# Kernel tuning notes

Hardware: AMD Instinct MI355X
Metric: run time of the kernel (lower is better)

## Reference

```python
import jax, jax.numpy as jnp
import numpy as np

DIM = 512
BATCH, SEQ = 4, 4096


def setup_inputs() -> dict:
    key = jax.random.key(0)
    kx, kq, kk, kv, ko = jax.random.split(key, 5)
    s = DIM ** -0.5  # fan-in style init scale for stability
    return {
        "x": jax.random.normal(kx, (BATCH, SEQ, DIM), dtype=jnp.float32),
        "Wq": jax.random.normal(kq, (DIM, DIM), dtype=jnp.float32) * s,
        "Wk": jax.random.normal(kk, (DIM, DIM), dtype=jnp.float32) * s,
        "Wv": jax.random.normal(kv, (DIM, DIM), dtype=jnp.float32) * s,
        "Wo": jax.random.normal(ko, (DIM, DIM), dtype=jnp.float32) * s,
    }


def reference(x, Wq, Wk, Wv, Wo):
    # x: [B, S, D]; projections (torch Linear, no bias -> x @ W here)
    q = jnp.einsum('bsd,dk->bsk', x, Wq)  # [B,S,K]
    k = jnp.einsum('bsd,dk->bsk', x, Wk)  # [B,S,K]
    v = jnp.einsum('bsd,dv->bsv', x, Wv)  # [B,S,V]

    # sequential recurrence: M_t = M_{t-1} + v_t k_t^T ; y_t = M_t q_t
    def step(M, qkv_t):
        q_t, k_t, v_t = qkv_t  # each [B, K] / [B, V]
        M = M + v_t[:, :, None] * k_t[:, None, :]  # [B, V, K]
        y_t = jnp.einsum('bvk,bk->bv', M, q_t)
        return M, y_t

    M0 = jnp.zeros((x.shape[0], Wv.shape[1], Wk.shape[1]), dtype=x.dtype)
    qT = jnp.swapaxes(q, 0, 1)  # [S,B,K]
    kT = jnp.swapaxes(k, 0, 1)
    vT = jnp.swapaxes(v, 0, 1)
    _, ys = jax.lax.scan(step, M0, (qT, kT, vT))  # ys: [S,B,V]
    y = jnp.swapaxes(ys, 0, 1)  # [B,S,V]
    return jnp.einsum('bsv,vd->bsd', y, Wo)
```

## Files before the change

### kernel.cpp

```cpp
#include <hip/hip_runtime.h>
#include <hip/hip_bf16.h>

typedef __attribute__((ext_vector_type(8))) short bf16x8;
typedef __attribute__((ext_vector_type(4))) float f32x4;

__device__ inline short f2bf(float f) {
    __hip_bfloat16 h = __float2bfloat16(f);
    short s;
    __builtin_memcpy(&s, &h, 2);
    return s;
}
__device__ inline float bf2f(short s) {
    unsigned int u = ((unsigned int)(unsigned short)s) << 16;
    float f;
    __builtin_memcpy(&f, &u, 4);
    return f;
}

__device__ inline void cp16_async(const void* g, void* l) {
    __builtin_amdgcn_global_load_lds(
        (const __attribute__((address_space(1))) void*)g,
        (__attribute__((address_space(3))) void*)l, 16, 0, 0);
}

__global__ void prep_kernel(const float* __restrict__ x, short* __restrict__ Xb,
                            const float* __restrict__ W0, const float* __restrict__ W1,
                            const float* __restrict__ W2, const float* __restrict__ W3,
                            short* __restrict__ W4T) {
    __shared__ short sT[64][72];
    const int bid = blockIdx.x, tid = threadIdx.x;
    if (bid < 8192) {
        int i = bid * 256 + tid;
        float4 f = ((const float4*)x)[i];
        union { short s[4]; int2 v; } u;
        u.s[0] = f2bf(f.x); u.s[1] = f2bf(f.y); u.s[2] = f2bf(f.z); u.s[3] = f2bf(f.w);
        ((int2*)Xb)[i] = u.v;
        return;
    }
    const int wb = bid - 8192;
    const int w = wb >> 6, r = wb & 63;
    const int n0 = (r >> 3) * 64, k0 = (r & 7) * 64;
    const float* W = (w == 0) ? W0 : (w == 1) ? W1 : (w == 2) ? W2 : W3;
#pragma unroll
    for (int rr = 0; rr < 4; ++rr) {
        int c = rr * 256 + tid;
        int row = c >> 4, col4 = (c & 15) * 4;
        float4 f = *(const float4*)&W[(size_t)(k0 + row) * 512 + n0 + col4];
        sT[col4 + 0][row] = f2bf(f.x);
        sT[col4 + 1][row] = f2bf(f.y);
        sT[col4 + 2][row] = f2bf(f.z);
        sT[col4 + 3][row] = f2bf(f.w);
    }
    __syncthreads();
#pragma unroll
    for (int rr = 0; rr < 2; ++rr) {
        int c = rr * 256 + tid;
        int f = c >> 3, k8 = (c & 7) * 8;
        int4 v = *(const int4*)&sT[f][k8];
        *(int4*)&W4T[(size_t)w * 262144 + (size_t)(n0 + f) * 512 + k0 + k8] = v;
    }
}


#define LDS_DBUF __shared__ short sA[8192], sB[8192]

__device__ inline void mfma_kloop_dbuf(const short* __restrict__ A, int lda,
                                       const short* __restrict__ B, int ldb,
                                       int Kd, f32x4* acc,
                                       short* sA, short* sB) {
    const int tid = threadIdx.x, lane = tid & 63, wv = tid >> 6;
    const int quad = lane >> 4, lr = lane & 15;
    const int wr = (wv >> 1) * 64, wc = (wv & 1) * 64;
    const int c0 = tid, c1 = tid + 256;
    const int r0 = c0 >> 2, k80 = (c0 & 3) * 8;
    const int r1 = c1 >> 2, k81 = (c1 & 3) * 8;

    __syncthreads();
    cp16_async(A + (size_t)r0 * lda + k80, sA + c0 * 8);
    cp16_async(A + (size_t)r1 * lda + k81, sA + c1 * 8);
    cp16_async(B + (size_t)r0 * ldb + k80, sB + c0 * 8);
    cp16_async(B + (size_t)r1 * ldb + k81, sB + c1 * 8);

    int cur = 0;
    for (int k0 = 0; k0 < Kd; k0 += 32) {
        __syncthreads();
        const int nxt = cur ^ 1;
        if (k0 + 32 < Kd) {
            const short* An = A + k0 + 32;
            const short* Bn = B + k0 + 32;
            cp16_async(An + (size_t)r0 * lda + k80, sA + nxt * 4096 + c0 * 8);
            cp16_async(An + (size_t)r1 * lda + k81, sA + nxt * 4096 + c1 * 8);
            cp16_async(Bn + (size_t)r0 * ldb + k80, sB + nxt * 4096 + c0 * 8);
            cp16_async(Bn + (size_t)r1 * ldb + k81, sB + nxt * 4096 + c1 * 8);
        }
        const short* pa = sA + cur * 4096;
        const short* pb = sB + cur * 4096;
        bf16x8 af[4], bfr[4];
#pragma unroll
        for (int i = 0; i < 4; ++i)
            af[i] = *(const bf16x8*)&pa[(wr + i * 16 + lr) * 32 + quad * 8];
#pragma unroll
        for (int j = 0; j < 4; ++j)
            bfr[j] = *(const bf16x8*)&pb[(wc + j * 16 + lr) * 32 + quad * 8];
#pragma unroll
        for (int i = 0; i < 4; ++i)
#pragma unroll
            for (int j = 0; j < 4; ++j)
                acc[i * 4 + j] = __builtin_amdgcn_mfma_f32_16x16x32_bf16(af[i], bfr[j], acc[i * 4 + j], 0, 0, 0);
        cur = nxt;
    }
}

__device__ inline void store_out(float* p, float v) { *p = v; }
__device__ inline void store_out(short* p, float v) { *p = f2bf(v); }

template <typename OutT>
__device__ inline void store_tile128(OutT* C, int ldc, const f32x4* acc) {
    const int lane = threadIdx.x & 63, wv = threadIdx.x >> 6;
    const int quad = lane >> 4, lr = lane & 15;
    const int wr = (wv >> 1) * 64, wc = (wv & 1) * 64;
#pragma unroll
    for (int i = 0; i < 4; ++i)
#pragma unroll
        for (int j = 0; j < 4; ++j)
#pragma unroll
            for (int r = 0; r < 4; ++r)
                store_out(&C[(size_t)(wr + i * 16 + quad * 4 + r) * ldc + wc + j * 16 + lr],
                          acc[i * 4 + j][r]);
}

__global__ __launch_bounds__(256, 2) void proj_all(const short* __restrict__ Xb,
                                                   const short* __restrict__ W4T,
                                                   short* __restrict__ Qb, short* __restrict__ Kb,
                                                   short* __restrict__ Vt, short* __restrict__ Kt) {
    LDS_DBUF;
    f32x4 acc[16];
#pragma unroll
    for (int i = 0; i < 16; ++i) acc[i] = (f32x4){0.f, 0.f, 0.f, 0.f};
    const int bid = blockIdx.x;
    const int lane = threadIdx.x & 63, wv = threadIdx.x >> 6;
    const int quad = lane >> 4, lr = lane & 15;
    const int wr = (wv >> 1) * 64, wc = (wv & 1) * 64;
    if (bid < 1024) {
        const int mt = bid >> 3, by = bid & 7;
        const short* At = Xb + (size_t)mt * 128 * 512;
        const short* Bt = W4T + (size_t)by * 128 * 512;
        short* Ct = ((by < 4) ? Qb : Kb) + (size_t)mt * 128 * 512 + (by & 3) * 128;
        mfma_kloop_dbuf(At, 512, Bt, 512, 512, acc, sA, sB);
        store_tile128(Ct, 512, acc);
        if (by >= 4) {
            const int b = mt >> 5;
            const int t0b = (mt & 31) * 128;
            const int f0 = (by - 4) * 128;
#pragma unroll
            for (int i = 0; i < 4; ++i)
#pragma unroll
                for (int j = 0; j < 4; ++j) {
                    int f = f0 + wc + j * 16 + lr;
                    int tt0 = t0b + wr + i * 16 + quad * 4;
                    short tmp[4];
#pragma unroll
                    for (int r = 0; r < 4; ++r) tmp[r] = f2bf(acc[i * 4 + j][r]);
                    *(int2*)&Kt[((size_t)b * 512 + f) * 4096 + tt0] = *(const int2*)tmp;
                }
        }
    } else {
        const int r = bid - 1024;
        const int b = r & 3, tt = (r >> 2) & 31, ft = r >> 7;
        const short* At = W4T + (size_t)2 * 262144 + (size_t)ft * 128 * 512;
        const short* Bt = Xb + ((size_t)b * 4096 + tt * 128) * 512;
        short* Ct = Vt + (size_t)b * 512 * 4096 + (size_t)ft * 128 * 4096 + tt * 128;
        mfma_kloop_dbuf(At, 512, Bt, 512, 512, acc, sA, sB);
        store_tile128(Ct, 4096, acc);
    }
}

__global__ __launch_bounds__(256, 2) void phaseA_k(const short* __restrict__ Vt,
                                                   const short* __restrict__ Kt,
                                                   short* __restrict__ AM) {
    LDS_DBUF;
    const int vb = blockIdx.x;
    const int xt = vb & 3, yt = (vb >> 2) & 3, bc = vb >> 4;
    const int b = bc >> 4, c = bc & 15;
    const short* Ap = Vt + ((size_t)b * 512 + xt * 128) * 4096 + c * 256;
    const short* Bp = Kt + ((size_t)b * 512 + yt * 128) * 4096 + c * 256;
    short* Cp = AM + (size_t)bc * 262144 + (size_t)xt * 128 * 512 + yt * 128;
    f32x4 acc[16];
#pragma unroll
    for (int i = 0; i < 16; ++i) acc[i] = (f32x4){0.f, 0.f, 0.f, 0.f};
    mfma_kloop_dbuf(Ap, 4096, Bp, 4096, 256, acc, sA, sB);
    store_tile128(Cp, 512, acc);
}

__global__ __launch_bounds__(256, 2) void scan_phaseS_k(short* __restrict__ AM,
                                                        const short* __restrict__ Q,
                                                        const short* __restrict__ K,
                                                        short* __restrict__ P) {
    LDS_DBUF;
    const int tid = threadIdx.x;
    if (blockIdx.x < 512) {
        int i = blockIdx.x * 256 + tid;
        int b = i >> 15;
        int vk8 = i & 32767;
        size_t base = (size_t)b * 16 * 262144 + (size_t)vk8 * 8;
        float acc[8];
#pragma unroll
        for (int s = 0; s < 8; ++s) acc[s] = 0.f;
        for (int c = 0; c < 16; ++c) {
            short* p = AM + base + (size_t)c * 262144;
            short in8[8];
            *(int4*)in8 = *(const int4*)p;
            short out8[8];
#pragma unroll
            for (int s = 0; s < 8; ++s) out8[s] = f2bf(acc[s]);
            *(int4*)p = *(const int4*)out8;
#pragma unroll
            for (int s = 0; s < 8; ++s) acc[s] += bf2f(in8[s]);
        }
        return;
    }
    const int e = blockIdx.x - 512;
    const int bc = e >> 2, mt = e & 1, nt = (e >> 1) & 1;
    if (mt < nt) return;
    const int b = bc >> 4, c = bc & 15;
    short* Pt = P + (size_t)bc * 65536 + (size_t)mt * 128 * 256 + nt * 128;
    const short* Ap = Q + ((size_t)(b * 4096 + c * 256 + mt * 128)) * 512;
    const short* Bp = K + ((size_t)(b * 4096 + c * 256 + nt * 128)) * 512;
    f32x4 acc[16];
#pragma unroll
    for (int i = 0; i < 16; ++i) acc[i] = (f32x4){0.f, 0.f, 0.f, 0.f};
    mfma_kloop_dbuf(Ap, 512, Bp, 512, 512, acc, sA, sB);
    const int lane = tid & 63, wv = tid >> 6;
    const int quad = lane >> 4, lr = lane & 15;
    const int wr = (wv >> 1) * 64, wc = (wv & 1) * 64;
    const bool diag = (mt == nt);
#pragma unroll
    for (int i = 0; i < 4; ++i)
#pragma unroll
        for (int j = 0; j < 4; ++j)
#pragma unroll
            for (int r = 0; r < 4; ++r) {
                int t = wr + i * 16 + quad * 4 + r;
                int jj = wc + j * 16 + lr;
                float v = (!diag || jj <= t) ? acc[i * 4 + j][r] : 0.f;
                Pt[(size_t)t * 256 + jj] = f2bf(v);
            }
}

__global__ __launch_bounds__(256, 2) void phaseY_k(const short* __restrict__ Q,
                                                   const short* __restrict__ Mpre,
                                                   const short* __restrict__ P,
                                                   const short* __restrict__ Vt,
                                                   short* __restrict__ Y) {
    LDS_DBUF;
    const int vb = blockIdx.x;
    const int mt = vb & 1, nt = (vb >> 1) & 3, bc = vb >> 3;
    const int b = bc >> 4, c = bc & 15;
    f32x4 acc[16];
#pragma unroll
    for (int i = 0; i < 16; ++i) acc[i] = (f32x4){0.f, 0.f, 0.f, 0.f};
    const short* Ai = Q + ((size_t)(b * 4096 + c * 256 + mt * 128)) * 512;
    const short* Bi = Mpre + (size_t)bc * 262144 + (size_t)nt * 128 * 512;
    mfma_kloop_dbuf(Ai, 512, Bi, 512, 512, acc, sA, sB);
    const short* Ap = P + (size_t)bc * 65536 + (size_t)mt * 128 * 256;
    const short* Bv = Vt + ((size_t)b * 512 + nt * 128) * 4096 + c * 256;
    mfma_kloop_dbuf(Ap, 256, Bv, 4096, (mt + 1) * 128, acc, sA, sB);
    short* Cp = Y + ((size_t)(b * 4096 + c * 256 + mt * 128)) * 512 + nt * 128;
    store_tile128(Cp, 512, acc);
}

__global__ __launch_bounds__(256, 2) void outproj_k(const short* __restrict__ Y,
                                                    const short* __restrict__ W4T,
                                                    float* __restrict__ out) {
    LDS_DBUF;
    const int mt = blockIdx.x >> 2, nt = blockIdx.x & 3;
    const short* At = Y + (size_t)mt * 128 * 512;
    const short* Bt = W4T + (size_t)3 * 262144 + (size_t)nt * 128 * 512;
    float* Ct = out + (size_t)mt * 128 * 512 + nt * 128;
    f32x4 acc[16];
#pragma unroll
    for (int i = 0; i < 16; ++i) acc[i] = (f32x4){0.f, 0.f, 0.f, 0.f};
    mfma_kloop_dbuf(At, 512, Bt, 512, 512, acc, sA, sB);
    store_tile128(Ct, 512, acc);
}


extern "C" void kernel_launch(void* const* d_in, const int* in_sizes, int n_in,
                              void* d_out, int out_size, void* d_ws, size_t ws_size,
                              hipStream_t stream) {
    const float* x  = (const float*)d_in[0];
    const float* Wq = (const float*)d_in[1];
    const float* Wk = (const float*)d_in[2];
    const float* Wv = (const float*)d_in[3];
    const float* Wo = (const float*)d_in[4];
    float* out = (float*)d_out;

    const size_t NTD = 16384 * 512;

    short* ws  = (short*)d_ws;
    short* Xb  = ws;
    short* Qb  = Xb + NTD;
    short* Kb  = Qb + NTD;
    short* Kt  = Kb + NTD;
    short* Vt  = Kt + NTD;
    short* P   = Vt + NTD;
    short* W4T = P + 4194304;
    short* AM  = W4T + 1048576;
    short* Yb  = Kb;

    prep_kernel<<<8448, 256, 0, stream>>>(x, Xb, Wq, Wk, Wv, Wo, W4T);
    proj_all<<<1536, 256, 0, stream>>>(Xb, W4T, Qb, Kb, Vt, Kt);
    phaseA_k<<<1024, 256, 0, stream>>>(Vt, Kt, AM);
    scan_phaseS_k<<<768, 256, 0, stream>>>(AM, Qb, Kb, P);
    phaseY_k<<<512, 256, 0, stream>>>(Qb, AM, P, Vt, Yb);
    outproj_k<<<512, 256, 0, stream>>>(Yb, W4T, out);
}
```

Baseline: 233.9 us.

## Replace double-buffered K loop with four-panel 128-wide K staging

After: 237.6 us. About the same (+1.6%).

```diff
diff --git a/kernel.cpp b/kernel.cpp
--- a/kernel.cpp
+++ b/kernel.cpp
@@ -62,12 +62,12 @@
 }
 
 
-#define LDS_DBUF __shared__ short sA[8192], sB[8192]
-
-__device__ inline void mfma_kloop_dbuf(const short* __restrict__ A, int lda,
-                                       const short* __restrict__ B, int ldb,
-                                       int Kd, f32x4* acc,
-                                       short* sA, short* sB) {
+#define LDS_P4 __shared__ short sA[4][4096], sB[4][4096]
+
+__device__ inline void mfma_kloop128(const short* __restrict__ A, int lda,
+                                     const short* __restrict__ B, int ldb,
+                                     int Kd, f32x4* acc,
+                                     short (*sA)[4096], short (*sB)[4096]) {
     const int tid = threadIdx.x, lane = tid & 63, wv = tid >> 6;
     const int quad = lane >> 4, lr = lane & 15;
     const int wr = (wv >> 1) * 64, wc = (wv & 1) * 64;
@@ -75,39 +75,35 @@
     const int r0 = c0 >> 2, k80 = (c0 & 3) * 8;
     const int r1 = c1 >> 2, k81 = (c1 & 3) * 8;
 
-    __syncthreads();
-    cp16_async(A + (size_t)r0 * lda + k80, sA + c0 * 8);
-    cp16_async(A + (size_t)r1 * lda + k81, sA + c1 * 8);
-    cp16_async(B + (size_t)r0 * ldb + k80, sB + c0 * 8);
-    cp16_async(B + (size_t)r1 * ldb + k81, sB + c1 * 8);
-
-    int cur = 0;
-    for (int k0 = 0; k0 < Kd; k0 += 32) {
+    for (int k0 = 0; k0 < Kd; k0 += 128) {
         __syncthreads();
-        const int nxt = cur ^ 1;
-        if (k0 + 32 < Kd) {
-            const short* An = A + k0 + 32;
-            const short* Bn = B + k0 + 32;
-            cp16_async(An + (size_t)r0 * lda + k80, sA + nxt * 4096 + c0 * 8);
-            cp16_async(An + (size_t)r1 * lda + k81, sA + nxt * 4096 + c1 * 8);
-            cp16_async(Bn + (size_t)r0 * ldb + k80, sB + nxt * 4096 + c0 * 8);
-            cp16_async(Bn + (size_t)r1 * ldb + k81, sB + nxt * 4096 + c1 * 8);
+#pragma unroll
+        for (int p = 0; p < 4; ++p) {
+            const short* Apnl = A + k0 + p * 32;
+            const short* Bpnl = B + k0 + p * 32;
+            cp16_async(Apnl + (size_t)r0 * lda + k80, sA[p] + c0 * 8);
+            cp16_async(Apnl + (size_t)r1 * lda + k81, sA[p] + c1 * 8);
+            cp16_async(Bpnl + (size_t)r0 * ldb + k80, sB[p] + c0 * 8);
+            cp16_async(Bpnl + (size_t)r1 * ldb + k81, sB[p] + c1 * 8);
         }
-        const short* pa = sA + cur * 4096;
-        const short* pb = sB + cur * 4096;
-        bf16x8 af[4], bfr[4];
-#pragma unroll
-        for (int i = 0; i < 4; ++i)
-            af[i] = *(const bf16x8*)&pa[(wr + i * 16 + lr) * 32 + quad * 8];
-#pragma unroll
-        for (int j = 0; j < 4; ++j)
-            bfr[j] = *(const bf16x8*)&pb[(wc + j * 16 + lr) * 32 + quad * 8];
-#pragma unroll
-        for (int i = 0; i < 4; ++i)
+        __syncthreads();
+#pragma unroll
+        for (int p = 0; p < 4; ++p) {
+            const short* pa = sA[p];
+            const short* pb = sB[p];
+            bf16x8 af[4], bfr[4];
+#pragma unroll
+            for (int i = 0; i < 4; ++i)
+                af[i] = *(const bf16x8*)&pa[(wr + i * 16 + lr) * 32 + quad * 8];
 #pragma unroll
             for (int j = 0; j < 4; ++j)
-                acc[i * 4 + j] = __builtin_amdgcn_mfma_f32_16x16x32_bf16(af[i], bfr[j], acc[i * 4 + j], 0, 0, 0);
-        cur = nxt;
+                bfr[j] = *(const bf16x8*)&pb[(wc + j * 16 + lr) * 32 + quad * 8];
+#pragma unroll
+            for (int i = 0; i < 4; ++i)
+#pragma unroll
+                for (int j = 0; j < 4; ++j)
+                    acc[i * 4 + j] = __builtin_amdgcn_mfma_f32_16x16x32_bf16(af[i], bfr[j], acc[i * 4 + j], 0, 0, 0);
+        }
     }
 }
 
@@ -133,7 +129,7 @@
                                                    const short* __restrict__ W4T,
                                                    short* __restrict__ Qb, short* __restrict__ Kb,
                                                    short* __restrict__ Vt, short* __restrict__ Kt) {
-    LDS_DBUF;
+    LDS_P4;
     f32x4 acc[16];
 #pragma unroll
     for (int i = 0; i < 16; ++i) acc[i] = (f32x4){0.f, 0.f, 0.f, 0.f};
@@ -146,7 +142,7 @@
         const short* At = Xb + (size_t)mt * 128 * 512;
         const short* Bt = W4T + (size_t)by * 128 * 512;
         short* Ct = ((by < 4) ? Qb : Kb) + (size_t)mt * 128 * 512 + (by & 3) * 128;
-        mfma_kloop_dbuf(At, 512, Bt, 512, 512, acc, sA, sB);
+        mfma_kloop128(At, 512, Bt, 512, 512, acc, sA, sB);
         store_tile128(Ct, 512, acc);
         if (by >= 4) {
             const int b = mt >> 5;
@@ -170,7 +166,7 @@
         const short* At = W4T + (size_t)2 * 262144 + (size_t)ft * 128 * 512;
         const short* Bt = Xb + ((size_t)b * 4096 + tt * 128) * 512;
         short* Ct = Vt + (size_t)b * 512 * 4096 + (size_t)ft * 128 * 4096 + tt * 128;
-        mfma_kloop_dbuf(At, 512, Bt, 512, 512, acc, sA, sB);
+        mfma_kloop128(At, 512, Bt, 512, 512, acc, sA, sB);
         store_tile128(Ct, 4096, acc);
     }
 }
@@ -178,7 +174,7 @@
 __global__ __launch_bounds__(256, 2) void phaseA_k(const short* __restrict__ Vt,
                                                    const short* __restrict__ Kt,
                                                    short* __restrict__ AM) {
-    LDS_DBUF;
+    LDS_P4;
     const int vb = blockIdx.x;
     const int xt = vb & 3, yt = (vb >> 2) & 3, bc = vb >> 4;
     const int b = bc >> 4, c = bc & 15;
@@ -188,7 +184,7 @@
     f32x4 acc[16];
 #pragma unroll
     for (int i = 0; i < 16; ++i) acc[i] = (f32x4){0.f, 0.f, 0.f, 0.f};
-    mfma_kloop_dbuf(Ap, 4096, Bp, 4096, 256, acc, sA, sB);
+    mfma_kloop128(Ap, 4096, Bp, 4096, 256, acc, sA, sB);
     store_tile128(Cp, 512, acc);
 }
 
@@ -196,7 +192,7 @@
                                                         const short* __restrict__ Q,
                                                         const short* __restrict__ K,
                                                         short* __restrict__ P) {
-    LDS_DBUF;
+    LDS_P4;
     const int tid = threadIdx.x;
     if (blockIdx.x < 512) {
         int i = blockIdx.x * 256 + tid;
@@ -229,7 +225,7 @@
     f32x4 acc[16];
 #pragma unroll
     for (int i = 0; i < 16; ++i) acc[i] = (f32x4){0.f, 0.f, 0.f, 0.f};
-    mfma_kloop_dbuf(Ap, 512, Bp, 512, 512, acc, sA, sB);
+    mfma_kloop128(Ap, 512, Bp, 512, 512, acc, sA, sB);
     const int lane = tid & 63, wv = tid >> 6;
     const int quad = lane >> 4, lr = lane & 15;
     const int wr = (wv >> 1) * 64, wc = (wv & 1) * 64;
@@ -252,7 +248,7 @@
                                                    const short* __restrict__ P,
                                                    const short* __restrict__ Vt,
                                                    short* __restrict__ Y) {
-    LDS_DBUF;
+    LDS_P4;
     const int vb = blockIdx.x;
     const int mt = vb & 1, nt = (vb >> 1) & 3, bc = vb >> 3;
     const int b = bc >> 4, c = bc & 15;
@@ -261,10 +257,10 @@
     for (int i = 0; i < 16; ++i) acc[i] = (f32x4){0.f, 0.f, 0.f, 0.f};
     const short* Ai = Q + ((size_t)(b * 4096 + c * 256 + mt * 128)) * 512;
     const short* Bi = Mpre + (size_t)bc * 262144 + (size_t)nt * 128 * 512;
-    mfma_kloop_dbuf(Ai, 512, Bi, 512, 512, acc, sA, sB);
+    mfma_kloop128(Ai, 512, Bi, 512, 512, acc, sA, sB);
     const short* Ap = P + (size_t)bc * 65536 + (size_t)mt * 128 * 256;
     const short* Bv = Vt + ((size_t)b * 512 + nt * 128) * 4096 + c * 256;
-    mfma_kloop_dbuf(Ap, 256, Bv, 4096, (mt + 1) * 128, acc, sA, sB);
+    mfma_kloop128(Ap, 256, Bv, 4096, (mt + 1) * 128, acc, sA, sB);
     short* Cp = Y + ((size_t)(b * 4096 + c * 256 + mt * 128)) * 512 + nt * 128;
     store_tile128(Cp, 512, acc);
 }
@@ -272,7 +268,7 @@
 __global__ __launch_bounds__(256, 2) void outproj_k(const short* __restrict__ Y,
                                                     const short* __restrict__ W4T,
                                                     float* __restrict__ out) {
-    LDS_DBUF;
+    LDS_P4;
     const int mt = blockIdx.x >> 2, nt = blockIdx.x & 3;
     const short* At = Y + (size_t)mt * 128 * 512;
     const short* Bt = W4T + (size_t)3 * 262144 + (size_t)nt * 128 * 512;
@@ -280,7 +276,7 @@
     f32x4 acc[16];
 #pragma unroll
     for (int i = 0; i < 16; ++i) acc[i] = (f32x4){0.f, 0.f, 0.f, 0.f};
-    mfma_kloop_dbuf(At, 512, Bt, 512, 512, acc, sA, sB);
+    mfma_kloop128(At, 512, Bt, 512, 512, acc, sA, sB);
     store_tile128(Ct, 512, acc);
 }
 
```
